# Performance work log

Measured on AMD Instinct MI355X. Metric: run time of the kernel, lower is better.

Reference implementation:

```python
import jax, jax.numpy as jnp
import numpy as np

N_NODES = 10000
N_EDGES = 50000
IN_F = 1433
OUT_F = 256
EPSILON = 8.0
SENSITIVITY = 1.0
DELTA = 1e-5
# total noise = sum of 3 independent per-share Gaussian draws
SIGMA = np.sqrt(3.0) * np.sqrt(2.0 * np.log(1.25 / DELTA)) * SENSITIVITY / EPSILON


def setup_inputs() -> dict:
    key = jax.random.key(0)
    k1, k2, k3, k4, k5, k6 = jax.random.split(key, 6)
    input_features = jax.random.normal(k1, (N_NODES, IN_F), dtype=jnp.float32)
    dst = jax.random.randint(k2, (N_EDGES,), 0, N_NODES)
    # src in [0, N_NODES]; value == N_NODES is the zero-vector sentinel
    src = jax.random.randint(k3, (N_EDGES,), 0, N_NODES + 1)
    edges = jnp.stack([dst, src], axis=1).astype(jnp.int64)
    stdv = 1.0 / np.sqrt(OUT_F)
    weight = jax.random.uniform(k4, (IN_F, OUT_F), minval=-stdv, maxval=stdv, dtype=jnp.float32)
    bias = jax.random.uniform(k5, (OUT_F,), minval=-stdv, maxval=stdv, dtype=jnp.float32)
    noise = jax.random.normal(k6, (N_NODES, IN_F), dtype=jnp.float32) * jnp.float32(SIGMA)
    return {"input_features": input_features, "edges": edges, "weight": weight,
            "bias": bias, "noise": noise}


def reference(input_features, edges, weight, bias, noise):
    n = input_features.shape[0]
    dst = edges[:, 0]
    src = edges[:, 1]
    # gather per-edge source features; sentinel src == n -> zero vector
    valid = (src < n)[:, None]                                   # [E,1]
    gathered = jnp.where(valid, input_features[jnp.clip(src, 0, n - 1)], 0.0)  # [E,F]
    # three secret shares sum exactly back to the value; the per-key aggregation
    # of each share then summed equals a single segment-sum over destinations
    agg = jax.ops.segment_sum(gathered, dst, num_segments=n)      # [N,F]
    # DP noise added to each share -> total noise added to the sum
    agg = agg + noise
    # torch.nn.functional.normalize(p=2, dim=1) with eps=1e-12
    norm = jnp.maximum(jnp.linalg.norm(agg, axis=1, keepdims=True), 1e-12)
    normed = agg / norm
    return normed @ weight + bias
```

## Files before the change

kernel.cpp:

```cpp
#include <hip/hip_runtime.h>
#include <math.h>

#define N_NODES 10000
#define N_EDGES 50000
#define IN_F    1433
#define OUT_F   256
#define GK      1440
#define NCHUNK  180
#define GM2     10112

typedef __bf16 bf16x8 __attribute__((ext_vector_type(8)));
typedef float  f32x4  __attribute__((ext_vector_type(4)));

typedef __attribute__((address_space(3))) unsigned int lds_u32;
typedef __attribute__((address_space(1))) unsigned int glb_u32;

__device__ __forceinline__ void stage16(const void* g, void* l) {
    __builtin_amdgcn_global_load_lds((glb_u32*)g, (lds_u32*)l, 16, 0, 0);
}


__global__ void k_hist(const int* __restrict__ edges, int* __restrict__ counts) {
    int e = blockIdx.x * blockDim.x + threadIdx.x;
    if (e < N_EDGES) {
        int dst = edges[2 * e];
        int src = edges[2 * e + 1];
        if (src < N_NODES) atomicAdd(&counts[dst], 1);
    }
}

__global__ void __launch_bounds__(1024) k_scan(const int* __restrict__ counts,
                                               int* __restrict__ offsets,
                                               int* __restrict__ cursor) {
    __shared__ int wsum[16];
    __shared__ int carry_s;
    const int t = threadIdx.x, lane = t & 63, wid = t >> 6;
    if (t == 0) carry_s = 0;
    __syncthreads();
    for (int base = 0; base < N_NODES; base += 1024) {
        int i = base + t;
        int v = (i < N_NODES) ? counts[i] : 0;
        int s = v;
#pragma unroll
        for (int off = 1; off < 64; off <<= 1) {
            int u = __shfl_up(s, off, 64);
            if (lane >= off) s += u;
        }
        if (lane == 63) wsum[wid] = s;
        __syncthreads();
        if (t == 0) {
            int run = carry_s;
#pragma unroll
            for (int w2 = 0; w2 < 16; ++w2) { int tmp = wsum[w2]; wsum[w2] = run; run += tmp; }
            carry_s = run;
        }
        __syncthreads();
        int excl = wsum[wid] + s - v;
        if (i < N_NODES) { offsets[i] = excl; cursor[i] = excl; }
        __syncthreads();
    }
    if (t == 0) offsets[N_NODES] = carry_s;
}

__global__ void k_fill(const int* __restrict__ edges, int* __restrict__ cursor,
                       int* __restrict__ edge_src) {
    int e = blockIdx.x * blockDim.x + threadIdx.x;
    if (e < N_EDGES) {
        int dst = edges[2 * e];
        int src = edges[2 * e + 1];
        if (src < N_NODES) {
            int pos = atomicAdd(&cursor[dst], 1);
            edge_src[pos] = src;
        }
    }
}


__global__ void __launch_bounds__(256) k_conv(const float* __restrict__ X,
                                              __bf16* __restrict__ Xbf) {
    const int t = threadIdx.x;
    const int w = t >> 6, lane = t & 63;
    const int r = blockIdx.x * 4 + w;
    const size_t rowf = (size_t)r * IN_F;
    __bf16* orow = Xbf + (size_t)r * GK;
    const int d = r & 3;

    f32x4 A[3][3];
#pragma unroll
    for (int s2 = 0; s2 < 3; ++s2) {
        int k = lane + s2 * 64;
        int kc = (k > 178) ? 178 : k;
        size_t q0 = (rowf + (size_t)kc * 8) >> 2;
        A[s2][0] = ((const f32x4*)X)[q0];
        A[s2][1] = ((const f32x4*)X)[q0 + 1];
        A[s2][2] = ((const f32x4*)X)[q0 + 2];
    }

#pragma unroll
    for (int s2 = 0; s2 < 3; ++s2) {
        int k = lane + s2 * 64;
        float q[12];
        *(f32x4*)&q[0] = A[s2][0];
        *(f32x4*)&q[4] = A[s2][1];
        *(f32x4*)&q[8] = A[s2][2];
        if (k < 179) {
            bf16x8 v;
            switch (d) {
            case 0:
#pragma unroll
                for (int j = 0; j < 8; ++j) v[j] = (__bf16)q[0 + j];
                break;
            case 1:
#pragma unroll
                for (int j = 0; j < 8; ++j) v[j] = (__bf16)q[1 + j];
                break;
            case 2:
#pragma unroll
                for (int j = 0; j < 8; ++j) v[j] = (__bf16)q[2 + j];
                break;
            default:
#pragma unroll
                for (int j = 0; j < 8; ++j) v[j] = (__bf16)q[3 + j];
                break;
            }
            *(bf16x8*)(orow + k * 8) = v;
        } else if (k == 179) {
            bf16x8 v;
            v[0] = (__bf16)q[8 + d];
#pragma unroll
            for (int j = 1; j < 8; ++j) v[j] = (__bf16)0.0f;
            *(bf16x8*)(orow + 1432) = v;
        }
    }
}


#define PREP_W  (OUT_F * GK)

__global__ void k_prep(const float* __restrict__ W, __bf16* __restrict__ BT) {
    int i = blockIdx.x * blockDim.x + threadIdx.x;
    if (i < PREP_W) {
        int n = i / GK, k = i % GK;
        BT[i] = (__bf16)((k < IN_F) ? W[(size_t)k * OUT_F + n] : 0.0f);
    }
}


__global__ void __launch_bounds__(192) k_agg(const __bf16* __restrict__ Xbf,
                                             const float* __restrict__ noise,
                                             const int* __restrict__ offsets,
                                             const int* __restrict__ edge_src,
                                             __bf16* __restrict__ aggbf,
                                             float* __restrict__ rnorm) {
    __shared__ float red[3];
    const int node = blockIdx.x;
    const int t = threadIdx.x;
    const bool active = (t < NCHUNK);
    const size_t co = (size_t)t * 8;

    if (node >= N_NODES) {
        if (active) {
            bf16x8 z;
#pragma unroll
            for (int j = 0; j < 8; ++j) z[j] = (__bf16)0.0f;
            *(bf16x8*)(aggbf + (size_t)node * GK + co) = z;
        }
        return;
    }

    const size_t nrowf = (size_t)node * IN_F;
    const int d = node & 3;
    f32x4 na, nb, nc;
    if (active) {
        int kc = (t > 178) ? 178 : t;
        size_t q0 = (nrowf + (size_t)kc * 8) >> 2;
        na = ((const f32x4*)noise)[q0];
        nb = ((const f32x4*)noise)[q0 + 1];
        nc = ((const f32x4*)noise)[q0 + 2];
    }

    const int beg = offsets[node], end = offsets[node + 1];

    float acc[8] = {0.f, 0.f, 0.f, 0.f, 0.f, 0.f, 0.f, 0.f};

    int kk = beg;
    for (; kk + 3 < end; kk += 4) {
        int n0 = edge_src[kk], n1 = edge_src[kk + 1];
        int n2 = edge_src[kk + 2], n3 = edge_src[kk + 3];
        if (active) {
            bf16x8 v0 = *(const bf16x8*)(Xbf + (size_t)n0 * GK + co);
            bf16x8 v1 = *(const bf16x8*)(Xbf + (size_t)n1 * GK + co);
            bf16x8 v2 = *(const bf16x8*)(Xbf + (size_t)n2 * GK + co);
            bf16x8 v3 = *(const bf16x8*)(Xbf + (size_t)n3 * GK + co);
#pragma unroll
            for (int j = 0; j < 8; ++j)
                acc[j] += ((float)v0[j] + (float)v1[j]) + ((float)v2[j] + (float)v3[j]);
        }
    }
    for (; kk < end; ++kk) {
        int n0 = edge_src[kk];
        if (active) {
            bf16x8 v = *(const bf16x8*)(Xbf + (size_t)n0 * GK + co);
#pragma unroll
            for (int j = 0; j < 8; ++j) acc[j] += (float)v[j];
        }
    }

    if (active) {
        float nq[12];
        *(f32x4*)&nq[0] = na; *(f32x4*)&nq[4] = nb; *(f32x4*)&nq[8] = nc;
        if (t < 179) {
            switch (d) {
            case 0:
#pragma unroll
                for (int j = 0; j < 8; ++j) acc[j] += nq[0 + j];
                break;
            case 1:
#pragma unroll
                for (int j = 0; j < 8; ++j) acc[j] += nq[1 + j];
                break;
            case 2:
#pragma unroll
                for (int j = 0; j < 8; ++j) acc[j] += nq[2 + j];
                break;
            default:
#pragma unroll
                for (int j = 0; j < 8; ++j) acc[j] += nq[3 + j];
                break;
            }
        } else {
            acc[0] += nq[8 + d];
        }
    }

    float ss = 0.f;
    if (active) {
        bf16x8 o;
#pragma unroll
        for (int j = 0; j < 8; ++j) { o[j] = (__bf16)acc[j]; ss += acc[j] * acc[j]; }
        *(bf16x8*)(aggbf + (size_t)node * GK + co) = o;
    }
    for (int off = 32; off > 0; off >>= 1) ss += __shfl_down(ss, off, 64);
    if ((t & 63) == 0) red[t >> 6] = ss;
    __syncthreads();
    if (t == 0)
        rnorm[node] = 1.0f / fmaxf(sqrtf(red[0] + red[1] + red[2]), 1e-12f);
}


#define BK 32

__global__ void __launch_bounds__(256) k_gemm(const __bf16* __restrict__ A,
                                              const __bf16* __restrict__ BT,
                                              const float* __restrict__ rnorm,
                                              const float* __restrict__ bias,
                                              float* __restrict__ out) {
    __shared__ __align__(16) __bf16 Asm[128][BK];
    __shared__ __align__(16) __bf16 Bsm[64][BK];

    const int t = threadIdx.x;
    const int lane = t & 63;
    const int w = t >> 6;
    const int row0 = blockIdx.y * 128;
    const int col0 = blockIdx.x * 64;

    const int sm = t >> 2;
    const int sc = (t & 3) * 8;

    f32x4 acc[2][4];
#pragma unroll
    for (int i = 0; i < 2; ++i)
#pragma unroll
        for (int j = 0; j < 4; ++j) acc[i][j] = (f32x4){0.f, 0.f, 0.f, 0.f};

    __bf16* asm0 = (__bf16*)Asm;
    __bf16* bsm0 = (__bf16*)Bsm;

#pragma unroll
    for (int r = 0; r < 2; ++r)
        stage16(A + (size_t)(row0 + sm + r * 64) * GK + sc, asm0 + r * 2048 + t * 8);
    stage16(BT + (size_t)(col0 + sm) * GK + sc, bsm0 + t * 8);

    const int kq = (lane >> 4) * 8;
    const int l15 = lane & 15;

    for (int kt = 0; kt < GK / BK; ++kt) {
        __syncthreads();

        bf16x8 af[2], bfr[4];
#pragma unroll
        for (int i = 0; i < 2; ++i) af[i]  = *(const bf16x8*)&Asm[w * 32 + i * 16 + l15][kq];
#pragma unroll
        for (int j = 0; j < 4; ++j) bfr[j] = *(const bf16x8*)&Bsm[j * 16 + l15][kq];

        __syncthreads();

        if (kt + 1 < GK / BK) {
            int k0 = (kt + 1) * BK;
#pragma unroll
            for (int r = 0; r < 2; ++r)
                stage16(A + (size_t)(row0 + sm + r * 64) * GK + k0 + sc, asm0 + r * 2048 + t * 8);
            stage16(BT + (size_t)(col0 + sm) * GK + k0 + sc, bsm0 + t * 8);
        }

#pragma unroll
        for (int i = 0; i < 2; ++i)
#pragma unroll
            for (int j = 0; j < 4; ++j)
                acc[i][j] = __builtin_amdgcn_mfma_f32_16x16x32_bf16(af[i], bfr[j], acc[i][j], 0, 0, 0);
    }

    const int rq4 = (lane >> 4) * 4;
#pragma unroll
    for (int i = 0; i < 2; ++i) {
        int gr0 = row0 + w * 32 + i * 16 + rq4;
#pragma unroll
        for (int r = 0; r < 4; ++r) {
            int gr = gr0 + r;
            if (gr < N_NODES) {
                float rn = rnorm[gr];
#pragma unroll
                for (int j = 0; j < 4; ++j) {
                    int gc = col0 + j * 16 + l15;
                    out[(size_t)gr * OUT_F + gc] = acc[i][j][r] * rn + bias[gc];
                }
            }
        }
    }
}


extern "C" void kernel_launch(void* const* d_in, const int* in_sizes, int n_in,
                              void* d_out, int out_size, void* d_ws, size_t ws_size,
                              hipStream_t stream) {
    const float* feat  = (const float*)d_in[0];
    const int*   edges = (const int*)d_in[1];
    const float* W     = (const float*)d_in[2];
    const float* bias  = (const float*)d_in[3];
    const float* noise = (const float*)d_in[4];
    float* out = (float*)d_out;

    char* ws = (char*)d_ws;
    size_t off = 0;
    auto carve = [&](size_t bytes) {
        void* p = ws + off;
        off = (off + bytes + 255) & ~(size_t)255;
        return p;
    };
    __bf16* Xbf     = (__bf16*)carve((size_t)N_NODES * GK * sizeof(__bf16));
    __bf16* aggbf   = (__bf16*)carve((size_t)GM2 * GK * sizeof(__bf16));
    __bf16* WbfT    = (__bf16*)carve((size_t)OUT_F * GK * sizeof(__bf16));
    float*  rnorm   = (float*)carve((size_t)N_NODES * sizeof(float));
    int*    counts  = (int*)carve((size_t)(N_NODES + 1) * sizeof(int));
    int*    offsets = (int*)carve((size_t)(N_NODES + 1) * sizeof(int));
    int*    cursor  = (int*)carve((size_t)(N_NODES + 1) * sizeof(int));
    int*    edge_src= (int*)carve((size_t)N_EDGES * sizeof(int));
    (void)ws_size;

    const int TB = 256;
    hipMemsetAsync(counts, 0, (size_t)(N_NODES + 1) * sizeof(int), stream);
    k_hist<<<(N_EDGES + TB - 1) / TB, TB, 0, stream>>>(edges, counts);
    k_scan<<<1, 1024, 0, stream>>>(counts, offsets, cursor);
    k_fill<<<(N_EDGES + TB - 1) / TB, TB, 0, stream>>>(edges, cursor, edge_src);

    k_conv<<<N_NODES / 4, 256, 0, stream>>>(feat, Xbf);

    k_prep<<<(PREP_W + TB - 1) / TB, TB, 0, stream>>>(W, WbfT);

    k_agg<<<GM2, 192, 0, stream>>>(Xbf, noise, offsets, edge_src, aggbf, rnorm);

    dim3 ggrid(OUT_F / 64, GM2 / 128);
    k_gemm<<<ggrid, 256, 0, stream>>>(aggbf, WbfT, rnorm, bias, out);
}
```

Measured before the change: 215.9 us.

## Fuse CSR build, feature conversion and weight prep into one kernel

Replaces the memset plus the histogram, scan, fill, convert and weight-prep launches with a single kernel. Block 0 builds the CSR in shared memory (count, scan, fill with LDS atomics), while the other blocks do the bf16 feature conversion and weight transpose concurrently. This removes several launch gaps and global atomics. The cost is that the serial CSR build runs on one block over all 50k edges, which may become the critical path, and it uses 40 KB of LDS per block, which may limit occupancy for the conversion blocks.

Measured after the change: 360.4 us. 1.67x slower.

```diff
diff --git a/kernel.cpp b/kernel.cpp
--- a/kernel.cpp
+++ b/kernel.cpp
@@ -20,126 +20,131 @@
 }
 
 
-__global__ void k_hist(const int* __restrict__ edges, int* __restrict__ counts) {
-    int e = blockIdx.x * blockDim.x + threadIdx.x;
-    if (e < N_EDGES) {
-        int dst = edges[2 * e];
-        int src = edges[2 * e + 1];
-        if (src < N_NODES) atomicAdd(&counts[dst], 1);
-    }
-}
-
-__global__ void __launch_bounds__(1024) k_scan(const int* __restrict__ counts,
-                                               int* __restrict__ offsets,
-                                               int* __restrict__ cursor) {
-    __shared__ int wsum[16];
-    __shared__ int carry_s;
-    const int t = threadIdx.x, lane = t & 63, wid = t >> 6;
-    if (t == 0) carry_s = 0;
-    __syncthreads();
-    for (int base = 0; base < N_NODES; base += 1024) {
-        int i = base + t;
-        int v = (i < N_NODES) ? counts[i] : 0;
-        int s = v;
+#define PREP_W      (OUT_F * GK)
+#define CONV_BLKS   (N_NODES / 4)
+#define PREP_BLKS   (PREP_W / 256)
+#define PHASEA_BLKS (1 + CONV_BLKS + PREP_BLKS)
+
+__global__ void __launch_bounds__(256) k_phaseA(const float* __restrict__ X,
+                                                __bf16* __restrict__ Xbf,
+                                                const float* __restrict__ W,
+                                                __bf16* __restrict__ BT,
+                                                const int* __restrict__ edges,
+                                                int* __restrict__ offsets,
+                                                int* __restrict__ edge_src) {
+    __shared__ int cnt[N_NODES];
+    __shared__ int wtot[4];
+    const int t = threadIdx.x;
+    const int b = blockIdx.x;
+
+    if (b == 0) {
+        for (int i = t; i < N_NODES; i += 256) cnt[i] = 0;
+        __syncthreads();
+        for (int e = t; e < N_EDGES; e += 256) {
+            int dst = edges[2 * e];
+            int src = edges[2 * e + 1];
+            if ((unsigned)src < N_NODES) atomicAdd(&cnt[dst], 1);
+        }
+        __syncthreads();
+        const int lane = t & 63, wid = t >> 6;
+        const int base = t * 40;
+        int lsum = 0;
+        for (int j = 0; j < 40; ++j) {
+            int idx = base + j;
+            if (idx < N_NODES) lsum += cnt[idx];
+        }
+        int s = lsum;
 #pragma unroll
         for (int off = 1; off < 64; off <<= 1) {
             int u = __shfl_up(s, off, 64);
             if (lane >= off) s += u;
         }
-        if (lane == 63) wsum[wid] = s;
-        __syncthreads();
-        if (t == 0) {
-            int run = carry_s;
-#pragma unroll
-            for (int w2 = 0; w2 < 16; ++w2) { int tmp = wsum[w2]; wsum[w2] = run; run += tmp; }
-            carry_s = run;
-        }
-        __syncthreads();
-        int excl = wsum[wid] + s - v;
-        if (i < N_NODES) { offsets[i] = excl; cursor[i] = excl; }
-        __syncthreads();
-    }
-    if (t == 0) offsets[N_NODES] = carry_s;
-}
-
-__global__ void k_fill(const int* __restrict__ edges, int* __restrict__ cursor,
-                       int* __restrict__ edge_src) {
-    int e = blockIdx.x * blockDim.x + threadIdx.x;
-    if (e < N_EDGES) {
-        int dst = edges[2 * e];
-        int src = edges[2 * e + 1];
-        if (src < N_NODES) {
-            int pos = atomicAdd(&cursor[dst], 1);
-            edge_src[pos] = src;
-        }
-    }
-}
-
-
-__global__ void __launch_bounds__(256) k_conv(const float* __restrict__ X,
-                                              __bf16* __restrict__ Xbf) {
-    const int t = threadIdx.x;
-    const int w = t >> 6, lane = t & 63;
-    const int r = blockIdx.x * 4 + w;
-    const size_t rowf = (size_t)r * IN_F;
-    __bf16* orow = Xbf + (size_t)r * GK;
-    const int d = r & 3;
-
-    f32x4 A[3][3];
-#pragma unroll
-    for (int s2 = 0; s2 < 3; ++s2) {
-        int k = lane + s2 * 64;
-        int kc = (k > 178) ? 178 : k;
-        size_t q0 = (rowf + (size_t)kc * 8) >> 2;
-        A[s2][0] = ((const f32x4*)X)[q0];
-        A[s2][1] = ((const f32x4*)X)[q0 + 1];
-        A[s2][2] = ((const f32x4*)X)[q0 + 2];
-    }
-
-#pragma unroll
-    for (int s2 = 0; s2 < 3; ++s2) {
-        int k = lane + s2 * 64;
-        float q[12];
-        *(f32x4*)&q[0] = A[s2][0];
-        *(f32x4*)&q[4] = A[s2][1];
-        *(f32x4*)&q[8] = A[s2][2];
-        if (k < 179) {
-            bf16x8 v;
-            switch (d) {
-            case 0:
-#pragma unroll
-                for (int j = 0; j < 8; ++j) v[j] = (__bf16)q[0 + j];
-                break;
-            case 1:
-#pragma unroll
-                for (int j = 0; j < 8; ++j) v[j] = (__bf16)q[1 + j];
-                break;
-            case 2:
-#pragma unroll
-                for (int j = 0; j < 8; ++j) v[j] = (__bf16)q[2 + j];
-                break;
-            default:
-#pragma unroll
-                for (int j = 0; j < 8; ++j) v[j] = (__bf16)q[3 + j];
-                break;
-            }
-            *(bf16x8*)(orow + k * 8) = v;
-        } else if (k == 179) {
-            bf16x8 v;
-            v[0] = (__bf16)q[8 + d];
-#pragma unroll
-            for (int j = 1; j < 8; ++j) v[j] = (__bf16)0.0f;
-            *(bf16x8*)(orow + 1432) = v;
-        }
-    }
-}
-
-
-#define PREP_W  (OUT_F * GK)
-
-__global__ void k_prep(const float* __restrict__ W, __bf16* __restrict__ BT) {
-    int i = blockIdx.x * blockDim.x + threadIdx.x;
-    if (i < PREP_W) {
+        if (lane == 63) wtot[wid] = s;
+        __syncthreads();
+        int carry = 0;
+        for (int w2 = 0; w2 < wid; ++w2) carry += wtot[w2];
+        int run = carry + s - lsum;
+        for (int j = 0; j < 40; ++j) {
+            int idx = base + j;
+            if (idx < N_NODES) {
+                int v = cnt[idx];
+                cnt[idx] = run;
+                offsets[idx] = run;
+                run += v;
+            }
+        }
+        if (t == 255) offsets[N_NODES] = run;
+        __syncthreads();
+        for (int e = t; e < N_EDGES; e += 256) {
+            int dst = edges[2 * e];
+            int src = edges[2 * e + 1];
+            if ((unsigned)src < N_NODES) {
+                int pos = atomicAdd(&cnt[dst], 1);
+                edge_src[pos] = src;
+            }
+        }
+        return;
+    }
+
+    if (b <= CONV_BLKS) {
+        const int w = t >> 6, lane = t & 63;
+        const int r = (b - 1) * 4 + w;
+        const size_t rowf = (size_t)r * IN_F;
+        __bf16* orow = Xbf + (size_t)r * GK;
+        const int d = r & 3;
+
+        f32x4 A[3][3];
+#pragma unroll
+        for (int s2 = 0; s2 < 3; ++s2) {
+            int k = lane + s2 * 64;
+            int kc = (k > 178) ? 178 : k;
+            size_t q0 = (rowf + (size_t)kc * 8) >> 2;
+            A[s2][0] = ((const f32x4*)X)[q0];
+            A[s2][1] = ((const f32x4*)X)[q0 + 1];
+            A[s2][2] = ((const f32x4*)X)[q0 + 2];
+        }
+
+#pragma unroll
+        for (int s2 = 0; s2 < 3; ++s2) {
+            int k = lane + s2 * 64;
+            float q[12];
+            *(f32x4*)&q[0] = A[s2][0];
+            *(f32x4*)&q[4] = A[s2][1];
+            *(f32x4*)&q[8] = A[s2][2];
+            if (k < 179) {
+                bf16x8 v;
+                switch (d) {
+                case 0:
+#pragma unroll
+                    for (int j = 0; j < 8; ++j) v[j] = (__bf16)q[0 + j];
+                    break;
+                case 1:
+#pragma unroll
+                    for (int j = 0; j < 8; ++j) v[j] = (__bf16)q[1 + j];
+                    break;
+                case 2:
+#pragma unroll
+                    for (int j = 0; j < 8; ++j) v[j] = (__bf16)q[2 + j];
+                    break;
+                default:
+#pragma unroll
+                    for (int j = 0; j < 8; ++j) v[j] = (__bf16)q[3 + j];
+                    break;
+                }
+                *(bf16x8*)(orow + k * 8) = v;
+            } else if (k == 179) {
+                bf16x8 v;
+                v[0] = (__bf16)q[8 + d];
+#pragma unroll
+                for (int j = 1; j < 8; ++j) v[j] = (__bf16)0.0f;
+                *(bf16x8*)(orow + 1432) = v;
+            }
+        }
+        return;
+    }
+
+    {
+        int i = (b - 1 - CONV_BLKS) * 256 + t;
         int n = i / GK, k = i % GK;
         BT[i] = (__bf16)((k < IN_F) ? W[(size_t)k * OUT_F + n] : 0.0f);
     }
@@ -351,21 +356,12 @@
     __bf16* aggbf   = (__bf16*)carve((size_t)GM2 * GK * sizeof(__bf16));
     __bf16* WbfT    = (__bf16*)carve((size_t)OUT_F * GK * sizeof(__bf16));
     float*  rnorm   = (float*)carve((size_t)N_NODES * sizeof(float));
-    int*    counts  = (int*)carve((size_t)(N_NODES + 1) * sizeof(int));
     int*    offsets = (int*)carve((size_t)(N_NODES + 1) * sizeof(int));
-    int*    cursor  = (int*)carve((size_t)(N_NODES + 1) * sizeof(int));
     int*    edge_src= (int*)carve((size_t)N_EDGES * sizeof(int));
     (void)ws_size;
 
-    const int TB = 256;
-    hipMemsetAsync(counts, 0, (size_t)(N_NODES + 1) * sizeof(int), stream);
-    k_hist<<<(N_EDGES + TB - 1) / TB, TB, 0, stream>>>(edges, counts);
-    k_scan<<<1, 1024, 0, stream>>>(counts, offsets, cursor);
-    k_fill<<<(N_EDGES + TB - 1) / TB, TB, 0, stream>>>(edges, cursor, edge_src);
-
-    k_conv<<<N_NODES / 4, 256, 0, stream>>>(feat, Xbf);
-
-    k_prep<<<(PREP_W + TB - 1) / TB, TB, 0, stream>>>(W, WbfT);
+    k_phaseA<<<PHASEA_BLKS, 256, 0, stream>>>(feat, Xbf, W, WbfT,
+                                              edges, offsets, edge_src);
 
     k_agg<<<GM2, 192, 0, stream>>>(Xbf, noise, offsets, edge_src, aggbf, rnorm);
 
```
